# Kernel optimization log

Hardware: AMD Instinct MI355X
Metric: run time of the kernel (lower is better)

The kernel has to match this reference:

```python
import jax, jax.numpy as jnp
import numpy as np

B, S, D = 4, 256, 768
DEP = 100
H, DK = 12, 64


def setup_inputs() -> dict:
    key = jax.random.key(0)
    ks = jax.random.split(key, 6)
    std_v = float(np.sqrt(2.0 / (D + D)))
    std_e = float(np.sqrt(2.0 / (DEP + DK)))
    return {
        "token_feature": jax.random.normal(ks[0], (B, S, D), dtype=jnp.float32),
        "edge_feature": jax.random.normal(ks[1], (B, S, S, DEP), dtype=jnp.float32),
        "dependency_masks": jax.random.randint(ks[2], (B, S, S), 0, 2, dtype=jnp.int32),
        "W_v": jax.random.normal(ks[3], (D, D), dtype=jnp.float32) * std_v,
        "W_e": jax.random.normal(ks[4], (DEP, D), dtype=jnp.float32) * std_e,
        "w_rel": jax.random.normal(ks[5], (DK,), dtype=jnp.float32) * (1.0 / np.sqrt(DK)),
    }


def reference(token_feature, edge_feature, dependency_masks, W_v, W_e, w_rel):
    b, s, d = token_feature.shape
    dk = w_rel.shape[0]
    h = d // dk
    # value projection per token j: [b, j, h, dk] (no need to replicate over i)
    V = (token_feature @ W_v).reshape(b, s, h, dk)
    # edge value per (i, j) pair: [b, i, j, h, dk]
    Ev = (edge_feature @ W_e).reshape(b, s, s, h, dk)
    # scalar score per (head, i, j): relu(Linear(dk -> 1))
    scores = jax.nn.relu(jnp.einsum("bijhd,d->bhij", Ev, w_rel))
    # mask: positions with dependency_masks == 0 get -1e6 (pre-softmax)
    scores = jnp.where(dependency_masks[:, None, :, :] == 0, jnp.float32(-1e6), scores)
    probs = jax.nn.softmax(scores, axis=-1)  # [b, h, i, j]; dropout = identity (eval)
    # weighted sum over neighbors j -> [b, i, h, dk] -> [b, s, d]
    ctx = jnp.einsum("bhij,bjhd->bihd", probs, V).reshape(b, s, d)
    return jax.nn.relu(token_feature + ctx)
```

## Files before the change

kernel.cpp:

```cpp
#include <hip/hip_runtime.h>
#include <math.h>

#define BB 4
#define SS 256
#define DD 768
#define DEPC 100
#define HH 12

typedef short bf16x8 __attribute__((ext_vector_type(8)));
typedef float f32x4 __attribute__((ext_vector_type(4)));

#define GLDS(gp, lp)                                                        \
    __builtin_amdgcn_global_load_lds(                                       \
        (const __attribute__((address_space(1))) void*)(gp),                \
        (__attribute__((address_space(3))) void*)(lp), 16, 0, 0)

__device__ __forceinline__ unsigned short f2bf(float x) {
    unsigned int u = __float_as_uint(x);
    u += 0x7FFF + ((u >> 16) & 1);
    return (unsigned short)(u >> 16);
}
__device__ __forceinline__ float bf2f(unsigned short h) {
    return __uint_as_float(((unsigned int)h) << 16);
}

__global__ __launch_bounds__(256) void k_prep(const float* __restrict__ W_e,
                                              const float* __restrict__ w_rel,
                                              const float* __restrict__ W_v,
                                              unsigned short* __restrict__ upk,
                                              unsigned short* __restrict__ wpk) {
    int t = threadIdx.x;
    if (blockIdx.x == 0) {
        __shared__ float u_l[HH][DEPC];
        const float4* wr = (const float4*)w_rel;
        float4 wrv[16];
#pragma unroll
        for (int c = 0; c < 16; ++c) wrv[c] = wr[c];
        for (int e = t; e < DEPC * HH; e += 256) {
            int p = e / HH, h = e % HH;
            const float4* we = (const float4*)(W_e + p * DD + h * 64);
            float acc = 0.f;
#pragma unroll
            for (int c = 0; c < 16; ++c) {
                float4 a = we[c], b = wrv[c];
                acc += a.x * b.x + a.y * b.y + a.z * b.z + a.w * b.w;
            }
            u_l[h][p] = acc;
        }
        __syncthreads();
        int s = t >> 6, l = t & 63;
        int h = l & 15, kg = l >> 4;
        unsigned short hi[8], lo[8];
#pragma unroll
        for (int e = 0; e < 8; ++e) {
            int k = 32 * s + kg * 8 + e;
            float v = (h < HH && k < DEPC) ? u_l[h][k] : 0.f;
            unsigned short hb = f2bf(v);
            hi[e] = hb;
            lo[e] = f2bf(v - bf2f(hb));
        }
        unsigned short* dh = upk + (s * 64 + l) * 8;
        unsigned short* dl = upk + 2048 + (s * 64 + l) * 8;
#pragma unroll
        for (int e = 0; e < 8; ++e) { dh[e] = hi[e]; dl[e] = lo[e]; }
    } else {
        int unit = (blockIdx.x - 1) * 4 + (t >> 6);
        int lane = t & 63;
        int s = unit / 48, ct = unit % 48;
        int cl = lane & 15, kg = lane >> 4;
        unsigned short hi[8], lo[8];
#pragma unroll
        for (int e = 0; e < 8; ++e) {
            int k = s * 32 + kg * 8 + e;
            float v = W_v[(size_t)k * DD + ct * 16 + cl];
            unsigned short hb = f2bf(v);
            hi[e] = hb;
            lo[e] = f2bf(v - bf2f(hb));
        }
        size_t base = ((size_t)(s * 48 + ct) * 64 + lane) * 8;
        unsigned short* dh = wpk + base;
        unsigned short* dl = wpk + 589824 + base;
#pragma unroll
        for (int e = 0; e < 8; ++e) { dh[e] = hi[e]; dl[e] = lo[e]; }
    }
}

__global__ __launch_bounds__(256) void k_v(const float* __restrict__ A,
                                           const unsigned short* __restrict__ wpk,
                                           unsigned short* __restrict__ Vbf) {
    __shared__ unsigned short Ah[2][32][40], Al[2][32][40];
    int t = threadIdx.x;
    int lane = t & 63, w = t >> 6;
    int wr = w >> 1, wc = w & 1;
    int r0 = blockIdx.x * 32, c0y = blockIdx.y;
    int srow = t >> 3, sq = t & 7;

    {
        float4 av = *(const float4*)&A[(size_t)(r0 + srow) * DD + 4 * sq];
        const float* af = (const float*)&av;
#pragma unroll
        for (int e = 0; e < 4; ++e) {
            unsigned short hb = f2bf(af[e]);
            Ah[0][srow][4 * sq + e] = hb;
            Al[0][srow][4 * sq + e] = f2bf(af[e] - bf2f(hb));
        }
    }
    __syncthreads();

    int ct = c0y * 2 + wc;
    int fr = wr * 16 + (lane & 15);
    int kg = lane >> 4;
    f32x4 acc = {0.f, 0.f, 0.f, 0.f};

    for (int s = 0; s < 24; ++s) {
        float4 nx = {0, 0, 0, 0};
        if (s + 1 < 24)
            nx = *(const float4*)&A[(size_t)(r0 + srow) * DD + (s + 1) * 32 + 4 * sq];

        const unsigned short* bp = wpk + ((size_t)(s * 48 + ct) * 64 + lane) * 8;
        bf16x8 bh = *(const bf16x8*)bp;
        bf16x8 bl = *(const bf16x8*)(bp + 589824);
        bf16x8 ah = *(const bf16x8*)&Ah[s & 1][fr][kg * 8];
        bf16x8 al = *(const bf16x8*)&Al[s & 1][fr][kg * 8];
        acc = __builtin_amdgcn_mfma_f32_16x16x32_bf16(ah, bh, acc, 0, 0, 0);
        acc = __builtin_amdgcn_mfma_f32_16x16x32_bf16(al, bh, acc, 0, 0, 0);
        acc = __builtin_amdgcn_mfma_f32_16x16x32_bf16(ah, bl, acc, 0, 0, 0);

        if (s + 1 < 24) {
            const float* nf = (const float*)&nx;
            int nb = (s + 1) & 1;
#pragma unroll
            for (int e = 0; e < 4; ++e) {
                unsigned short hb = f2bf(nf[e]);
                Ah[nb][srow][4 * sq + e] = hb;
                Al[nb][srow][4 * sq + e] = f2bf(nf[e] - bf2f(hb));
            }
        }
        __syncthreads();
    }

    int col = c0y * 32 + wc * 16 + (lane & 15);
    int rowb = r0 + wr * 16 + (lane >> 4) * 4;
#pragma unroll
    for (int e = 0; e < 4; ++e)
        Vbf[(size_t)(rowb + e) * DD + col] = f2bf(acc[e]);
}

__global__ __launch_bounds__(256) void k_sc(const float* __restrict__ edge,
                                            const int* __restrict__ mask,
                                            const unsigned short* __restrict__ upk,
                                            float* __restrict__ scores) {
    __shared__ float buf[64 * DEPC + 32];
    int t = threadIdx.x;
    int jc = blockIdx.x & 3;
    int i  = blockIdx.x >> 2;
    int b  = blockIdx.y;
    int lane = t & 63, w = t >> 6;

    const float* src = edge + (size_t)((b * SS + i) * SS + jc * 64) * DEPC;
    for (int call = w; call < 25; call += 4)
        GLDS(src + call * 256 + lane * 4, &buf[call * 256]);
    if (t < 32) buf[6400 + t] = 0.f;

    bf16x8 uh[4], ul[4];
#pragma unroll
    for (int s = 0; s < 4; ++s) {
        uh[s] = *(const bf16x8*)(upk + (s * 64 + lane) * 8);
        ul[s] = *(const bf16x8*)(upk + 2048 + (s * 64 + lane) * 8);
    }
    __syncthreads();

    int arow = lane & 15, kg = lane >> 4;
    const float* rbase = buf + (w * 16 + arow) * DEPC;
    f32x4 acc = {0.f, 0.f, 0.f, 0.f};
#pragma unroll
    for (int s = 0; s < 4; ++s) {
        const float4* p = (const float4*)(rbase + 32 * s + kg * 8);
        float4 va = p[0], vb = p[1];
        float ev[8] = {va.x, va.y, va.z, va.w, vb.x, vb.y, vb.z, vb.w};
        bf16x8 ehi, elo;
#pragma unroll
        for (int e = 0; e < 8; ++e) {
            unsigned short hb = f2bf(ev[e]);
            ehi[e] = (short)hb;
            elo[e] = (short)f2bf(ev[e] - bf2f(hb));
        }
        acc = __builtin_amdgcn_mfma_f32_16x16x32_bf16(ehi, uh[s], acc, 0, 0, 0);
        acc = __builtin_amdgcn_mfma_f32_16x16x32_bf16(ehi, ul[s], acc, 0, 0, 0);
        acc = __builtin_amdgcn_mfma_f32_16x16x32_bf16(elo, uh[s], acc, 0, 0, 0);
    }

    int h = lane & 15;
    int j0 = jc * 64 + w * 16 + (lane >> 4) * 4;
    int4 mk = *(const int4*)(mask + (size_t)(b * SS + i) * SS + j0);
    float4 r;
    r.x = mk.x ? fmaxf(acc[0], 0.f) : -1e6f;
    r.y = mk.y ? fmaxf(acc[1], 0.f) : -1e6f;
    r.z = mk.z ? fmaxf(acc[2], 0.f) : -1e6f;
    r.w = mk.w ? fmaxf(acc[3], 0.f) : -1e6f;
    if (h < HH)
        *(float4*)&scores[(((size_t)b * HH + h) * SS + i) * SS + j0] = r;
}

__global__ __launch_bounds__(256) void k_ctx(const float* __restrict__ scores,
                                             const unsigned short* __restrict__ Vbf,
                                             const float* __restrict__ token,
                                             float* __restrict__ out) {
    __shared__ float P[16][260];
    __shared__ unsigned short Pb[16][264];
    int t = threadIdx.x;
    int i0 = blockIdx.x * 16, h = blockIdx.y, b = blockIdx.z;
    int lane = t & 63, w = t >> 6;

    const float* sbase = scores + (((size_t)b * HH + h) * SS + i0) * SS;
#pragma unroll
    for (int k = 0; k < 4; ++k) {
        int idx = t + 256 * k;
        int r = idx >> 6, jc = idx & 63;
        float4 v = *(const float4*)(sbase + (size_t)r * SS + 4 * jc);
        *(float4*)&P[r][4 * jc] = v;
    }
    __syncthreads();

    for (int r = w; r < 16; r += 4) {
        float x0 = P[r][lane],       x1 = P[r][lane + 64];
        float x2 = P[r][lane + 128], x3 = P[r][lane + 192];
        float m = fmaxf(fmaxf(x0, x1), fmaxf(x2, x3));
#pragma unroll
        for (int o = 32; o > 0; o >>= 1) m = fmaxf(m, __shfl_xor(m, o, 64));
        x0 = __expf(x0 - m); x1 = __expf(x1 - m);
        x2 = __expf(x2 - m); x3 = __expf(x3 - m);
        float s = x0 + x1 + x2 + x3;
#pragma unroll
        for (int o = 32; o > 0; o >>= 1) s += __shfl_xor(s, o, 64);
        float inv = 1.0f / s;
        Pb[r][lane]       = f2bf(x0 * inv);
        Pb[r][lane + 64]  = f2bf(x1 * inv);
        Pb[r][lane + 128] = f2bf(x2 * inv);
        Pb[r][lane + 192] = f2bf(x3 * inv);
    }
    __syncthreads();

    int cl = lane & 15, kg = lane >> 4;
    f32x4 acc = {0.f, 0.f, 0.f, 0.f};
    const unsigned short* vb = Vbf + (size_t)b * SS * DD + h * 64 + w * 16 + cl;
#pragma unroll
    for (int s = 0; s < 8; ++s) {
        bf16x8 af = *(const bf16x8*)&Pb[cl][s * 32 + kg * 8];
        bf16x8 bfr;
#pragma unroll
        for (int e = 0; e < 8; ++e)
            bfr[e] = (short)vb[(size_t)(s * 32 + kg * 8 + e) * DD];
        acc = __builtin_amdgcn_mfma_f32_16x16x32_bf16(af, bfr, acc, 0, 0, 0);
    }

    int col = h * 64 + w * 16 + cl;
#pragma unroll
    for (int e = 0; e < 4; ++e) {
        size_t o = (size_t)(b * SS + i0 + kg * 4 + e) * DD + col;
        out[o] = fmaxf(token[o] + acc[e], 0.f);
    }
}

extern "C" void kernel_launch(void* const* d_in, const int* in_sizes, int n_in,
                              void* d_out, int out_size, void* d_ws, size_t ws_size,
                              hipStream_t stream) {
    const float* token = (const float*)d_in[0];
    const float* edge  = (const float*)d_in[1];
    const int*   mask  = (const int*)d_in[2];
    const float* W_v   = (const float*)d_in[3];
    const float* W_e   = (const float*)d_in[4];
    const float* w_rel = (const float*)d_in[5];
    float* out = (float*)d_out;

    char* ws = (char*)d_ws;
    unsigned short* upk = (unsigned short*)(ws);
    unsigned short* wpk = (unsigned short*)(ws + 8192);
    unsigned short* Vbf = (unsigned short*)(ws + 8192 + 2359296);
    float* scores = (float*)(ws + 8192 + 2359296 + 1572864 + 1024);

    hipLaunchKernelGGL(k_prep, dim3(289),       dim3(256), 0, stream, W_e, w_rel, W_v, upk, wpk);
    hipLaunchKernelGGL(k_v,    dim3(32, 24),    dim3(256), 0, stream, token, wpk, Vbf);
    hipLaunchKernelGGL(k_sc,   dim3(SS * 4, BB), dim3(256), 0, stream, edge, mask, upk, scores);
    hipLaunchKernelGGL(k_ctx,  dim3(16, HH, BB), dim3(256), 0, stream, scores, Vbf, token, out);
}
```

Baseline: 58.15 us.

## Merge V projection and score kernels into one launch with block specialization

Combines the independent value-projection GEMM and the edge-score kernel into a single launch. The first 192 x-blocks per batch row compute V tiles and the rest compute scores, with both sharing one shared-memory buffer. This drops one launch and lets the small V GEMM overlap with the bandwidth-bound score pass instead of running serially. In exchange, both branches now use the larger shared-memory allocation, which may reduce occupancy for the V blocks.

```diff
diff --git a/kernel.cpp b/kernel.cpp
--- a/kernel.cpp
+++ b/kernel.cpp
@@ -85,14 +85,18 @@
     }
 }
 
-__global__ __launch_bounds__(256) void k_v(const float* __restrict__ A,
-                                           const unsigned short* __restrict__ wpk,
-                                           unsigned short* __restrict__ Vbf) {
-    __shared__ unsigned short Ah[2][32][40], Al[2][32][40];
-    int t = threadIdx.x;
+__device__ __forceinline__ void body_v(char* smem, int unit, int t,
+                                       const float* __restrict__ A,
+                                       const unsigned short* __restrict__ wpk,
+                                       unsigned short* __restrict__ Vbf) {
+    unsigned short* Ah = (unsigned short*)smem;
+    unsigned short* Al = Ah + 2560;
+#define AH(bf, r, c) Ah[((bf) * 32 + (r)) * 40 + (c)]
+#define AL(bf, r, c) Al[((bf) * 32 + (r)) * 40 + (c)]
     int lane = t & 63, w = t >> 6;
     int wr = w >> 1, wc = w & 1;
-    int r0 = blockIdx.x * 32, c0y = blockIdx.y;
+    int vr = unit & 31, c0y = unit >> 5;
+    int r0 = vr * 32;
     int srow = t >> 3, sq = t & 7;
 
     {
@@ -101,8 +105,8 @@
 #pragma unroll
         for (int e = 0; e < 4; ++e) {
             unsigned short hb = f2bf(af[e]);
-            Ah[0][srow][4 * sq + e] = hb;
-            Al[0][srow][4 * sq + e] = f2bf(af[e] - bf2f(hb));
+            AH(0, srow, 4 * sq + e) = hb;
+            AL(0, srow, 4 * sq + e) = f2bf(af[e] - bf2f(hb));
         }
     }
     __syncthreads();
@@ -120,8 +124,8 @@
         const unsigned short* bp = wpk + ((size_t)(s * 48 + ct) * 64 + lane) * 8;
         bf16x8 bh = *(const bf16x8*)bp;
         bf16x8 bl = *(const bf16x8*)(bp + 589824);
-        bf16x8 ah = *(const bf16x8*)&Ah[s & 1][fr][kg * 8];
-        bf16x8 al = *(const bf16x8*)&Al[s & 1][fr][kg * 8];
+        bf16x8 ah = *(const bf16x8*)&AH(s & 1, fr, kg * 8);
+        bf16x8 al = *(const bf16x8*)&AL(s & 1, fr, kg * 8);
         acc = __builtin_amdgcn_mfma_f32_16x16x32_bf16(ah, bh, acc, 0, 0, 0);
         acc = __builtin_amdgcn_mfma_f32_16x16x32_bf16(al, bh, acc, 0, 0, 0);
         acc = __builtin_amdgcn_mfma_f32_16x16x32_bf16(ah, bl, acc, 0, 0, 0);
@@ -132,8 +136,8 @@
 #pragma unroll
             for (int e = 0; e < 4; ++e) {
                 unsigned short hb = f2bf(nf[e]);
-                Ah[nb][srow][4 * sq + e] = hb;
-                Al[nb][srow][4 * sq + e] = f2bf(nf[e] - bf2f(hb));
+                AH(nb, srow, 4 * sq + e) = hb;
+                AL(nb, srow, 4 * sq + e) = f2bf(nf[e] - bf2f(hb));
             }
         }
         __syncthreads();
@@ -144,17 +148,16 @@
 #pragma unroll
     for (int e = 0; e < 4; ++e)
         Vbf[(size_t)(rowb + e) * DD + col] = f2bf(acc[e]);
-}
-
-__global__ __launch_bounds__(256) void k_sc(const float* __restrict__ edge,
-                                            const int* __restrict__ mask,
-                                            const unsigned short* __restrict__ upk,
-                                            float* __restrict__ scores) {
-    __shared__ float buf[64 * DEPC + 32];
-    int t = threadIdx.x;
-    int jc = blockIdx.x & 3;
-    int i  = blockIdx.x >> 2;
-    int b  = blockIdx.y;
+#undef AH
+#undef AL
+}
+
+__device__ __forceinline__ void body_sc(char* smem, int jc, int i, int b, int t,
+                                        const float* __restrict__ edge,
+                                        const int* __restrict__ mask,
+                                        const unsigned short* __restrict__ upk,
+                                        float* __restrict__ scores) {
+    float* buf = (float*)smem;
     int lane = t & 63, w = t >> 6;
 
     const float* src = edge + (size_t)((b * SS + i) * SS + jc * 64) * DEPC;
@@ -202,6 +205,25 @@
         *(float4*)&scores[(((size_t)b * HH + h) * SS + i) * SS + j0] = r;
 }
 
+__global__ __launch_bounds__(256) void k_main(const float* __restrict__ token,
+                                              const unsigned short* __restrict__ wpk,
+                                              unsigned short* __restrict__ Vbf,
+                                              const float* __restrict__ edge,
+                                              const int* __restrict__ mask,
+                                              const unsigned short* __restrict__ upk,
+                                              float* __restrict__ scores) {
+    __shared__ __align__(16) char smem[25728];
+    int t = threadIdx.x;
+    int x = blockIdx.x, b = blockIdx.y;
+    if (x < 192) {
+        int unit = b * 192 + x;
+        body_v(smem, unit, t, token, wpk, Vbf);
+    } else {
+        int xx = x - 192;
+        body_sc(smem, xx & 3, xx >> 2, b, t, edge, mask, upk, scores);
+    }
+}
+
 __global__ __launch_bounds__(256) void k_ctx(const float* __restrict__ scores,
                                              const unsigned short* __restrict__ Vbf,
                                              const float* __restrict__ token,
@@ -279,8 +301,8 @@
     unsigned short* Vbf = (unsigned short*)(ws + 8192 + 2359296);
     float* scores = (float*)(ws + 8192 + 2359296 + 1572864 + 1024);
 
-    hipLaunchKernelGGL(k_prep, dim3(289),       dim3(256), 0, stream, W_e, w_rel, W_v, upk, wpk);
-    hipLaunchKernelGGL(k_v,    dim3(32, 24),    dim3(256), 0, stream, token, wpk, Vbf);
-    hipLaunchKernelGGL(k_sc,   dim3(SS * 4, BB), dim3(256), 0, stream, edge, mask, upk, scores);
-    hipLaunchKernelGGL(k_ctx,  dim3(16, HH, BB), dim3(256), 0, stream, scores, Vbf, token, out);
-}
+    hipLaunchKernelGGL(k_prep, dim3(289),             dim3(256), 0, stream, W_e, w_rel, W_v, upk, wpk);
+    hipLaunchKernelGGL(k_main, dim3(192 + SS * 4, BB), dim3(256), 0, stream,
+                       token, wpk, Vbf, edge, mask, upk, scores);
+    hipLaunchKernelGGL(k_ctx,  dim3(16, HH, BB),      dim3(256), 0, stream, scores, Vbf, token, out);
+}
```

Measured after the change: 54.98 us. 1.06x faster.
